# Kernel tuning notes

Hardware: AMD Instinct MI355X
Metric: run time of the kernel (lower is better)

## Reference

```python
import jax, jax.numpy as jnp
import numpy as np

EPS = 1e-8  # torch.cosine_similarity default eps


def setup_inputs() -> dict:
    key = jax.random.key(0)
    ks = jax.random.split(key, 6)
    B, U, P, H = 256, 128, 64, 768
    utt_output = jax.random.normal(ks[0], (U, B, H), dtype=jnp.float32)
    pheno_output = jax.random.normal(ks[1], (P, B, H), dtype=jnp.float32)
    # Conv1d(in=U, out=U, kernel=P) weight: [out, in, kernel]
    w_utt = jax.random.normal(ks[2], (U, U, P), dtype=jnp.float32) / np.sqrt(U * P)
    b_utt = jax.random.normal(ks[3], (U,), dtype=jnp.float32) * 0.01
    # Conv1d(in=P, out=P, kernel=U) weight: [out, in, kernel]
    w_pheno = jax.random.normal(ks[4], (P, P, U), dtype=jnp.float32) / np.sqrt(P * U)
    b_pheno = jax.random.normal(ks[5], (P,), dtype=jnp.float32) * 0.01
    return {"utt_output": utt_output, "pheno_output": pheno_output,
            "w_utt": w_utt, "b_utt": b_utt, "w_pheno": w_pheno, "b_pheno": b_pheno}


def reference(utt_output, pheno_output, w_utt, b_utt, w_pheno, b_pheno):
    # [len, B, H] -> [B, len, H]
    u = jnp.swapaxes(utt_output, 0, 1)    # [B, U, H]
    p = jnp.swapaxes(pheno_output, 0, 1)  # [B, P, H]
    # cosine similarity matrix c[b,i,j] = <u_i, p_j> / (max(|u_i|,eps)*max(|p_j|,eps))
    un = u / jnp.maximum(jnp.linalg.norm(u, axis=-1, keepdims=True), EPS)
    pn = p / jnp.maximum(jnp.linalg.norm(p, axis=-1, keepdims=True), EPS)
    c = jnp.einsum('buh,bph->bup', un, pn)  # [B, U, P]
    # Conv1d with kernel covering the full width -> output length 1, i.e. an einsum
    row_logits = jnp.einsum('bup,oup->bo', c, w_utt) + b_utt        # [B, U]
    col_logits = jnp.einsum('bup,opu->bo', c, w_pheno) + b_pheno    # [B, P]
    row_attention = jax.nn.softmax(row_logits, axis=-1)
    col_attention = jax.nn.softmax(col_logits, axis=-1)
    return row_attention, col_attention
```

## Files before the change

### kernel.cpp

```cpp
#include <hip/hip_runtime.h>
#include <stdint.h>

#define Bn 256
#define Un 128
#define Pn 64
#define Hn 768
#define Ototal 192
#define KC 16

typedef short s4v __attribute__((ext_vector_type(4)));
typedef short s8v __attribute__((ext_vector_type(8)));
typedef float f4v __attribute__((ext_vector_type(4)));

__device__ __forceinline__ short f2bf(float x) {
  union { float f; uint32_t u; } c; c.f = x;
  uint32_t r = (c.u + 0x7fffu + ((c.u >> 16) & 1u)) >> 16;
  return (short)(r & 0xffffu);
}

__global__ void __launch_bounds__(256) convW(const float* __restrict__ w_utt,
                                             const float* __restrict__ w_ph,
                                             ushort* __restrict__ Wbf) {
  int idx = blockIdx.x * 256 + threadIdx.x;
  int o = idx >> 13;
  int k = idx & 8191;
  float v;
  if (o < Un) {
    v = w_utt[(size_t)o * 8192 + k];
  } else {
    int oc = o - Un;
    int i = k >> 6, j = k & 63;
    v = w_ph[((size_t)oc * Pn + j) * Un + i];
  }
  Wbf[idx] = (ushort)f2bf(v);
}

__global__ void __launch_bounds__(512) phaseA(const float* __restrict__ utt,
                                              const float* __restrict__ ph,
                                              ushort* __restrict__ Cbf) {
  const int b = blockIdx.x;
  const int t = threadIdx.x;
  const int w = t >> 6, l = t & 63;

  __shared__ short uA[Un * 32];
  __shared__ short pB[Pn * 32];
  __shared__ float s_inu[Un];
  __shared__ float s_inp[Pn];

  const int r0   = t >> 3;
  const int hoff = (t & 7) * 4;
  const size_t rstride = (size_t)Bn * Hn;

  const float* ub = utt + (size_t)b * Hn;
  const float* pb = ph  + (size_t)b * Hn;

  float4 ru0, ru1, rp0;
  float ssu0 = 0.f, ssu1 = 0.f, ssp0 = 0.f;

  f4v zero4 = {0.f, 0.f, 0.f, 0.f};
  f4v acc[4] = {zero4, zero4, zero4, zero4};

  {
    const float* u0 = ub + (size_t)r0 * rstride + hoff;
    ru0 = *(const float4*)(u0);
    ru1 = *(const float4*)(u0 + (size_t)64 * rstride);
    rp0 = *(const float4*)(pb + (size_t)r0 * rstride + hoff);
  }

  const int m  = l & 15;
  const int ko = (l >> 4) * 8;
  const short* aptr = &uA[(16 * w + m) * 32 + ko];

  for (int c = 0; c < 24; ++c) {
    __syncthreads();
    ssu0 += ru0.x*ru0.x + ru0.y*ru0.y + ru0.z*ru0.z + ru0.w*ru0.w;
    ssu1 += ru1.x*ru1.x + ru1.y*ru1.y + ru1.z*ru1.z + ru1.w*ru1.w;
    ssp0 += rp0.x*rp0.x + rp0.y*rp0.y + rp0.z*rp0.z + rp0.w*rp0.w;
    s4v a0 = {f2bf(ru0.x), f2bf(ru0.y), f2bf(ru0.z), f2bf(ru0.w)};
    s4v a1 = {f2bf(ru1.x), f2bf(ru1.y), f2bf(ru1.z), f2bf(ru1.w)};
    s4v p0 = {f2bf(rp0.x), f2bf(rp0.y), f2bf(rp0.z), f2bf(rp0.w)};
    *(s4v*)&uA[(size_t)r0 * 32 + hoff]        = a0;
    *(s4v*)&uA[((size_t)r0 + 64) * 32 + hoff] = a1;
    *(s4v*)&pB[(size_t)r0 * 32 + hoff]        = p0;
    __syncthreads();
    if (c < 23) {
      const int hb = (c + 1) * 32 + hoff;
      const float* u0 = ub + (size_t)r0 * rstride + hb;
      ru0 = *(const float4*)(u0);
      ru1 = *(const float4*)(u0 + (size_t)64 * rstride);
      rp0 = *(const float4*)(pb + (size_t)r0 * rstride + hb);
    }
    s8v af = *(const s8v*)aptr;
#pragma unroll
    for (int jt = 0; jt < 4; ++jt) {
      s8v bf = *(const s8v*)&pB[(16 * jt + m) * 32 + ko];
      acc[jt] = __builtin_amdgcn_mfma_f32_16x16x32_bf16(af, bf, acc[jt], 0, 0, 0);
    }
  }

  ssu0 += __shfl_xor(ssu0, 4); ssu0 += __shfl_xor(ssu0, 2); ssu0 += __shfl_xor(ssu0, 1);
  ssu1 += __shfl_xor(ssu1, 4); ssu1 += __shfl_xor(ssu1, 2); ssu1 += __shfl_xor(ssu1, 1);
  ssp0 += __shfl_xor(ssp0, 4); ssp0 += __shfl_xor(ssp0, 2); ssp0 += __shfl_xor(ssp0, 1);
  if ((t & 7) == 0) {
    int row = t >> 3;
    s_inu[row]      = 1.f / fmaxf(sqrtf(ssu0), 1e-8f);
    s_inu[row + 64] = 1.f / fmaxf(sqrtf(ssu1), 1e-8f);
    s_inp[row]      = 1.f / fmaxf(sqrtf(ssp0), 1e-8f);
  }
  __syncthreads();

  const int cl = l & 15;
  const int rq = (l >> 4) * 4;
#pragma unroll
  for (int jt = 0; jt < 4; ++jt) {
    int j = 16 * jt + cl;
    float sj = s_inp[j];
#pragma unroll
    for (int r = 0; r < 4; ++r) {
      int il = 16 * w + rq + r;
      float v = acc[jt][r] * s_inu[il] * sj;
      Cbf[((size_t)b * Un + il) * Pn + j] = (ushort)f2bf(v);
    }
  }
}

__global__ void __launch_bounds__(256) phaseB(const ushort* __restrict__ Cbf,
                                              const ushort* __restrict__ Wbf,
                                              float* __restrict__ partial) {
  const int kc = blockIdx.x;
  const int mt = blockIdx.y;
  const int nt = blockIdx.z;
  const int t = threadIdx.x;
  const int w = t >> 6, l = t & 63;

  __shared__ short Ab[64 * 32];
  __shared__ short Bb[64 * 32];

  const int row = t >> 2;
  const int ko8 = (t & 3) * 8;

  f4v zero4 = {0.f, 0.f, 0.f, 0.f};
  f4v acc[4] = {zero4, zero4, zero4, zero4};

  const ushort* Ag = Cbf + (size_t)(mt * 64 + row) * 8192 + kc * 512 + ko8;
  const ushort* Bg = Wbf + (size_t)(nt * 64 + row) * 8192 + kc * 512 + ko8;
  const int m  = l & 15;
  const int ko = (l >> 4) * 8;

  for (int c = 0; c < 16; ++c) {
    s8v av = *(const s8v*)(Ag + c * 32);
    s8v bv = *(const s8v*)(Bg + c * 32);
    __syncthreads();
    *(s8v*)&Ab[row * 32 + ko8] = av;
    *(s8v*)&Bb[row * 32 + ko8] = bv;
    __syncthreads();
    s8v af = *(const s8v*)&Ab[(16 * w + m) * 32 + ko];
#pragma unroll
    for (int jt = 0; jt < 4; ++jt) {
      s8v bf = *(const s8v*)&Bb[(16 * jt + m) * 32 + ko];
      acc[jt] = __builtin_amdgcn_mfma_f32_16x16x32_bf16(af, bf, acc[jt], 0, 0, 0);
    }
  }

  const int rq = (l >> 4) * 4;
#pragma unroll
  for (int jt = 0; jt < 4; ++jt) {
    int og = nt * 64 + 16 * jt + (l & 15);
#pragma unroll
    for (int r = 0; r < 4; ++r) {
      int bg = mt * 64 + 16 * w + rq + r;
      partial[((size_t)kc * Bn + bg) * Ototal + og] = acc[jt][r];
    }
  }
}

__global__ void __launch_bounds__(192) phaseC(const float* __restrict__ partial,
                                              const float* __restrict__ b_utt,
                                              const float* __restrict__ b_ph,
                                              float* __restrict__ out) {
  const int b = blockIdx.x;
  const int t = threadIdx.x;
  const int w = t >> 6, l = t & 63;

  float v = 0.f;
#pragma unroll
  for (int kc = 0; kc < KC; ++kc)
    v += partial[((size_t)kc * Bn + b) * Ototal + t];
  v += (t < Un) ? b_utt[t] : b_ph[t - Un];

  __shared__ float red[3];
  float mx = v;
  for (int o = 32; o >= 1; o >>= 1) mx = fmaxf(mx, __shfl_xor(mx, o));
  if (l == 0) red[w] = mx;
  __syncthreads();
  float gmax = (t < Un) ? fmaxf(red[0], red[1]) : red[2];
  float e = expf(v - gmax);
  float s = e;
  for (int o = 32; o >= 1; o >>= 1) s += __shfl_xor(s, o);
  __syncthreads();
  if (l == 0) red[w] = s;
  __syncthreads();
  float gs = (t < Un) ? (red[0] + red[1]) : red[2];
  float r = e / gs;
  if (t < Un) out[(size_t)b * Un + t] = r;
  else        out[(size_t)Bn * Un + (size_t)b * Pn + (t - Un)] = r;
}

extern "C" void kernel_launch(void* const* d_in, const int* in_sizes, int n_in,
                              void* d_out, int out_size, void* d_ws, size_t ws_size,
                              hipStream_t stream) {
  const float* utt   = (const float*)d_in[0];
  const float* ph    = (const float*)d_in[1];
  const float* w_utt = (const float*)d_in[2];
  const float* b_utt = (const float*)d_in[3];
  const float* w_ph  = (const float*)d_in[4];
  const float* b_ph  = (const float*)d_in[5];

  char* ws = (char*)d_ws;
  ushort* Cbf     = (ushort*)(ws);
  ushort* Wbf     = (ushort*)(ws + 4194304);
  float*  partial = (float*)(ws + 7340032);

  convW <<<dim3(6144), dim3(256), 0, stream>>>(w_utt, w_ph, Wbf);
  phaseA<<<dim3(Bn),   dim3(512), 0, stream>>>(utt, ph, Cbf);
  phaseB<<<dim3(KC, 4, 3), dim3(256), 0, stream>>>(Cbf, Wbf, partial);
  phaseC<<<dim3(Bn),   dim3(192), 0, stream>>>(partial, b_utt, b_ph, (float*)d_out);
}
```

Before: 212.9 us.

## Double-buffer phaseA with wider chunks, 1024 threads, padded LDS, and tiled weight transpose

phaseA now runs 1024 threads per batch and processes 64-wide H chunks. It keeps two register prefetch stages and double-buffered LDS, so there is one barrier per chunk instead of two. LDS rows are padded (LDU/LDB) to reduce bank conflicts in phaseA and phaseB. convW transposes the pheno weights through a shared-memory tile, so the global reads are coalesced rather than strided. The aim is to hide global memory latency in the bandwidth-bound similarity pass, at the cost of more LDS and register pressure.

Measured after the change: 245.7 us. 1.15x slower.

```diff
diff --git a/kernel.cpp b/kernel.cpp
--- a/kernel.cpp
+++ b/kernel.cpp
@@ -8,6 +8,11 @@
 #define Ototal 192
 #define KC 16
 
+#define CH 64
+#define NCH 12
+#define LDU 72
+#define LDB 56
+
 typedef short s4v __attribute__((ext_vector_type(4)));
 typedef short s8v __attribute__((ext_vector_type(8)));
 typedef float f4v __attribute__((ext_vector_type(4)));
@@ -21,103 +26,128 @@
 __global__ void __launch_bounds__(256) convW(const float* __restrict__ w_utt,
                                              const float* __restrict__ w_ph,
                                              ushort* __restrict__ Wbf) {
-  int idx = blockIdx.x * 256 + threadIdx.x;
-  int o = idx >> 13;
-  int k = idx & 8191;
-  float v;
-  if (o < Un) {
-    v = w_utt[(size_t)o * 8192 + k];
-  } else {
-    int oc = o - Un;
+  __shared__ float tile[64 * 129];
+  const int bx = blockIdx.x;
+  const int t = threadIdx.x;
+  if (bx < 4096) {
+    int idx = bx * 256 + t;
+    Wbf[idx] = (ushort)f2bf(w_utt[idx]);
+    return;
+  }
+  const int oc = bx - 4096;
+  const float* src = w_ph + (size_t)oc * 8192;
+#pragma unroll
+  for (int itr = 0; itr < 8; ++itr) {
+    int idx = itr * 1024 + t * 4;
+    int j = idx >> 7, i = idx & 127;
+    float4 v = *(const float4*)(src + idx);
+    tile[j * 129 + i + 0] = v.x;
+    tile[j * 129 + i + 1] = v.y;
+    tile[j * 129 + i + 2] = v.z;
+    tile[j * 129 + i + 3] = v.w;
+  }
+  __syncthreads();
+  const size_t obase = (size_t)(128 + oc) * 8192;
+#pragma unroll
+  for (int itr = 0; itr < 8; ++itr) {
+    int k = itr * 1024 + t * 4;
     int i = k >> 6, j = k & 63;
-    v = w_ph[((size_t)oc * Pn + j) * Un + i];
-  }
-  Wbf[idx] = (ushort)f2bf(v);
-}
-
-__global__ void __launch_bounds__(512) phaseA(const float* __restrict__ utt,
-                                              const float* __restrict__ ph,
-                                              ushort* __restrict__ Cbf) {
+    s4v o4 = { f2bf(tile[(j + 0) * 129 + i]),
+               f2bf(tile[(j + 1) * 129 + i]),
+               f2bf(tile[(j + 2) * 129 + i]),
+               f2bf(tile[(j + 3) * 129 + i]) };
+    *(s4v*)&Wbf[obase + k] = o4;
+  }
+}
+
+__global__ void __launch_bounds__(1024, 4) phaseA(const float* __restrict__ utt,
+                                                  const float* __restrict__ ph,
+                                                  ushort* __restrict__ Cbf) {
   const int b = blockIdx.x;
   const int t = threadIdx.x;
   const int w = t >> 6, l = t & 63;
 
-  __shared__ short uA[Un * 32];
-  __shared__ short pB[Pn * 32];
+  __shared__ short uA[2][Un * LDU];
+  __shared__ short pB[2][Pn * LDU];
   __shared__ float s_inu[Un];
   __shared__ float s_inp[Pn];
 
-  const int r0   = t >> 3;
-  const int hoff = (t & 7) * 4;
+  const int ur = t >> 3;
+  const int uc = (t & 7) * 8;
+  const int pr = t >> 4;
+  const int pc = (t & 15) * 4;
+
   const size_t rstride = (size_t)Bn * Hn;
-
-  const float* ub = utt + (size_t)b * Hn;
-  const float* pb = ph  + (size_t)b * Hn;
-
-  float4 ru0, ru1, rp0;
-  float ssu0 = 0.f, ssu1 = 0.f, ssp0 = 0.f;
-
+  const float* ubase = utt + (size_t)b * Hn + (size_t)ur * rstride + uc;
+  const float* pbase = ph  + (size_t)b * Hn + (size_t)pr * rstride + pc;
+
+  float4 ru0[2], ru1[2], rp[2];
+#pragma unroll
+  for (int s = 0; s < 2; ++s) {
+    ru0[s] = *(const float4*)(ubase + s * CH);
+    ru1[s] = *(const float4*)(ubase + s * CH + 4);
+    rp[s]  = *(const float4*)(pbase + s * CH);
+  }
+
+  float ssu = 0.f, ssp = 0.f;
   f4v zero4 = {0.f, 0.f, 0.f, 0.f};
-  f4v acc[4] = {zero4, zero4, zero4, zero4};
-
-  {
-    const float* u0 = ub + (size_t)r0 * rstride + hoff;
-    ru0 = *(const float4*)(u0);
-    ru1 = *(const float4*)(u0 + (size_t)64 * rstride);
-    rp0 = *(const float4*)(pb + (size_t)r0 * rstride + hoff);
-  }
+  f4v acc[2] = {zero4, zero4};
 
   const int m  = l & 15;
   const int ko = (l >> 4) * 8;
-  const short* aptr = &uA[(16 * w + m) * 32 + ko];
-
-  for (int c = 0; c < 24; ++c) {
+  const int it = w & 7;
+  const int jp = w >> 3;
+
+  const int ua_w = ur * LDU + uc;
+  const int pb_w = pr * LDU + pc;
+
+#pragma unroll
+  for (int c = 0; c < NCH; ++c) {
+    const int s = c & 1;
+    float4 a0 = ru0[s], a1 = ru1[s], p0 = rp[s];
+    ssu += a0.x*a0.x + a0.y*a0.y + a0.z*a0.z + a0.w*a0.w
+         + a1.x*a1.x + a1.y*a1.y + a1.z*a1.z + a1.w*a1.w;
+    ssp += p0.x*p0.x + p0.y*p0.y + p0.z*p0.z + p0.w*p0.w;
+    if (c + 2 < NCH) {
+      ru0[s] = *(const float4*)(ubase + (c + 2) * CH);
+      ru1[s] = *(const float4*)(ubase + (c + 2) * CH + 4);
+      rp[s]  = *(const float4*)(pbase + (c + 2) * CH);
+    }
+    s8v au = { f2bf(a0.x), f2bf(a0.y), f2bf(a0.z), f2bf(a0.w),
+               f2bf(a1.x), f2bf(a1.y), f2bf(a1.z), f2bf(a1.w) };
+    s4v pp = { f2bf(p0.x), f2bf(p0.y), f2bf(p0.z), f2bf(p0.w) };
+    *(s8v*)&uA[s][ua_w] = au;
+    *(s4v*)&pB[s][pb_w] = pp;
     __syncthreads();
-    ssu0 += ru0.x*ru0.x + ru0.y*ru0.y + ru0.z*ru0.z + ru0.w*ru0.w;
-    ssu1 += ru1.x*ru1.x + ru1.y*ru1.y + ru1.z*ru1.z + ru1.w*ru1.w;
-    ssp0 += rp0.x*rp0.x + rp0.y*rp0.y + rp0.z*rp0.z + rp0.w*rp0.w;
-    s4v a0 = {f2bf(ru0.x), f2bf(ru0.y), f2bf(ru0.z), f2bf(ru0.w)};
-    s4v a1 = {f2bf(ru1.x), f2bf(ru1.y), f2bf(ru1.z), f2bf(ru1.w)};
-    s4v p0 = {f2bf(rp0.x), f2bf(rp0.y), f2bf(rp0.z), f2bf(rp0.w)};
-    *(s4v*)&uA[(size_t)r0 * 32 + hoff]        = a0;
-    *(s4v*)&uA[((size_t)r0 + 64) * 32 + hoff] = a1;
-    *(s4v*)&pB[(size_t)r0 * 32 + hoff]        = p0;
-    __syncthreads();
-    if (c < 23) {
-      const int hb = (c + 1) * 32 + hoff;
-      const float* u0 = ub + (size_t)r0 * rstride + hb;
-      ru0 = *(const float4*)(u0);
-      ru1 = *(const float4*)(u0 + (size_t)64 * rstride);
-      rp0 = *(const float4*)(pb + (size_t)r0 * rstride + hb);
-    }
-    s8v af = *(const s8v*)aptr;
-#pragma unroll
-    for (int jt = 0; jt < 4; ++jt) {
-      s8v bf = *(const s8v*)&pB[(16 * jt + m) * 32 + ko];
-      acc[jt] = __builtin_amdgcn_mfma_f32_16x16x32_bf16(af, bf, acc[jt], 0, 0, 0);
-    }
-  }
-
-  ssu0 += __shfl_xor(ssu0, 4); ssu0 += __shfl_xor(ssu0, 2); ssu0 += __shfl_xor(ssu0, 1);
-  ssu1 += __shfl_xor(ssu1, 4); ssu1 += __shfl_xor(ssu1, 2); ssu1 += __shfl_xor(ssu1, 1);
-  ssp0 += __shfl_xor(ssp0, 4); ssp0 += __shfl_xor(ssp0, 2); ssp0 += __shfl_xor(ssp0, 1);
-  if ((t & 7) == 0) {
-    int row = t >> 3;
-    s_inu[row]      = 1.f / fmaxf(sqrtf(ssu0), 1e-8f);
-    s_inu[row + 64] = 1.f / fmaxf(sqrtf(ssu1), 1e-8f);
-    s_inp[row]      = 1.f / fmaxf(sqrtf(ssp0), 1e-8f);
-  }
+    const short* ab = &uA[s][(it * 16 + m) * LDU + ko];
+    const short* bb = &pB[s][(jp * 32 + m) * LDU + ko];
+#pragma unroll
+    for (int ks = 0; ks < 2; ++ks) {
+      s8v af = *(const s8v*)(ab + ks * 32);
+#pragma unroll
+      for (int jt = 0; jt < 2; ++jt) {
+        s8v bf = *(const s8v*)(bb + jt * 16 * LDU + ks * 32);
+        acc[jt] = __builtin_amdgcn_mfma_f32_16x16x32_bf16(af, bf, acc[jt], 0, 0, 0);
+      }
+    }
+  }
+
+  ssu += __shfl_xor(ssu, 4); ssu += __shfl_xor(ssu, 2); ssu += __shfl_xor(ssu, 1);
+  ssp += __shfl_xor(ssp, 8); ssp += __shfl_xor(ssp, 4);
+  ssp += __shfl_xor(ssp, 2); ssp += __shfl_xor(ssp, 1);
+  if ((t & 7) == 0)  s_inu[ur] = 1.f / fmaxf(sqrtf(ssu), 1e-8f);
+  if ((t & 15) == 0) s_inp[pr] = 1.f / fmaxf(sqrtf(ssp), 1e-8f);
   __syncthreads();
 
   const int cl = l & 15;
   const int rq = (l >> 4) * 4;
 #pragma unroll
-  for (int jt = 0; jt < 4; ++jt) {
-    int j = 16 * jt + cl;
+  for (int jt = 0; jt < 2; ++jt) {
+    int j = jp * 32 + jt * 16 + cl;
     float sj = s_inp[j];
 #pragma unroll
     for (int r = 0; r < 4; ++r) {
-      int il = 16 * w + rq + r;
+      int il = it * 16 + rq + r;
       float v = acc[jt][r] * s_inu[il] * sj;
       Cbf[((size_t)b * Un + il) * Pn + j] = (ushort)f2bf(v);
     }
@@ -133,8 +163,8 @@
   const int t = threadIdx.x;
   const int w = t >> 6, l = t & 63;
 
-  __shared__ short Ab[64 * 32];
-  __shared__ short Bb[64 * 32];
+  __shared__ short Ab[64 * LDB];
+  __shared__ short Bb[64 * LDB];
 
   const int row = t >> 2;
   const int ko8 = (t & 3) * 8;
@@ -151,13 +181,13 @@
     s8v av = *(const s8v*)(Ag + c * 32);
     s8v bv = *(const s8v*)(Bg + c * 32);
     __syncthreads();
-    *(s8v*)&Ab[row * 32 + ko8] = av;
-    *(s8v*)&Bb[row * 32 + ko8] = bv;
+    *(s8v*)&Ab[row * LDB + ko8] = av;
+    *(s8v*)&Bb[row * LDB + ko8] = bv;
     __syncthreads();
-    s8v af = *(const s8v*)&Ab[(16 * w + m) * 32 + ko];
+    s8v af = *(const s8v*)&Ab[(16 * w + m) * LDB + ko];
 #pragma unroll
     for (int jt = 0; jt < 4; ++jt) {
-      s8v bf = *(const s8v*)&Bb[(16 * jt + m) * 32 + ko];
+      s8v bf = *(const s8v*)&Bb[(16 * jt + m) * LDB + ko];
       acc[jt] = __builtin_amdgcn_mfma_f32_16x16x32_bf16(af, bf, acc[jt], 0, 0, 0);
     }
   }
@@ -221,8 +251,8 @@
   ushort* Wbf     = (ushort*)(ws + 4194304);
   float*  partial = (float*)(ws + 7340032);
 
-  convW <<<dim3(6144), dim3(256), 0, stream>>>(w_utt, w_ph, Wbf);
-  phaseA<<<dim3(Bn),   dim3(512), 0, stream>>>(utt, ph, Cbf);
+  convW <<<dim3(4096 + 64), dim3(256), 0, stream>>>(w_utt, w_ph, Wbf);
+  phaseA<<<dim3(Bn), dim3(1024), 0, stream>>>(utt, ph, Cbf);
   phaseB<<<dim3(KC, 4, 3), dim3(256), 0, stream>>>(Cbf, Wbf, partial);
-  phaseC<<<dim3(Bn),   dim3(192), 0, stream>>>(partial, b_utt, b_ph, (float*)d_out);
-}
+  phaseC<<<dim3(Bn), dim3(192), 0, stream>>>(partial, b_utt, b_ph, (float*)d_out);
+}
```
